# Kernel optimization log

Hardware: AMD Instinct MI355X
Metric: run time of the kernel (lower is better)

Reference implementation:

```python
import jax, jax.numpy as jnp
import numpy as np

HIDDEN = 2048
NUM_HEADS = 16
HEAD_DIM = HIDDEN // NUM_HEADS  # 128
ROPE_BASE = 10000.0


def setup_inputs() -> dict:
    key = jax.random.key(0)
    ks = jax.random.split(key, 5)
    B, T, C = 2, 2048, HIDDEN
    scale = 1.0 / np.sqrt(C)
    x = jax.random.normal(ks[0], (B, T, C), dtype=jnp.float32)
    Wq = jax.random.normal(ks[1], (C, C), dtype=jnp.float32) * scale
    Wk = jax.random.normal(ks[2], (C, C), dtype=jnp.float32) * scale
    Wv = jax.random.normal(ks[3], (C, C), dtype=jnp.float32) * scale
    Wo = jax.random.normal(ks[4], (C, C), dtype=jnp.float32) * scale
    return {"x": x, "Wq": Wq, "Wk": Wk, "Wv": Wv, "Wo": Wo}


def _rope_cos_sin(T, dtype):
    # inv_freq: [D/2]; emb: [T, D] = cat(freqs, freqs)
    inv_freq = 1.0 / (ROPE_BASE ** (jnp.arange(0, HEAD_DIM, 2, dtype=jnp.float32) / HEAD_DIM))
    t = jnp.arange(T, dtype=jnp.float32)
    freqs = t[:, None] * inv_freq[None, :]          # [T, D/2]
    emb = jnp.concatenate([freqs, freqs], axis=-1)  # [T, D]
    # broadcast shape [1, T, 1, D] to match q/k [B, T, H, D]
    return jnp.cos(emb)[None, :, None, :].astype(dtype), jnp.sin(emb)[None, :, None, :].astype(dtype)


def _rotate_half(u):
    u1, u2 = jnp.split(u, 2, axis=-1)
    return jnp.concatenate([-u2, u1], axis=-1)


def reference(x, Wq, Wk, Wv, Wo):
    B, T, C = x.shape
    H, D = NUM_HEADS, HEAD_DIM
    # QKV projections (torch Linear: x @ W.T). Weights here stored as [C, C] so use x @ W.
    q = (x @ Wq).reshape(B, T, H, D)
    k = (x @ Wk).reshape(B, T, H, D)
    v = (x @ Wv).reshape(B, T, H, D)
    cos, sin = _rope_cos_sin(T, x.dtype)
    q = q * cos + _rotate_half(q) * sin
    k = k * cos + _rotate_half(k) * sin
    # causal SDPA: scores [B, H, T, T]
    scale = 1.0 / jnp.sqrt(jnp.asarray(D, dtype=x.dtype))
    scores = jnp.einsum('bqhd,bkhd->bhqk', q, k) * scale
    causal = jnp.tril(jnp.ones((T, T), dtype=bool))
    scores = jnp.where(causal[None, None, :, :], scores, jnp.asarray(-jnp.inf, dtype=scores.dtype))
    attn = jax.nn.softmax(scores, axis=-1)
    out = jnp.einsum('bhqk,bkhd->bqhd', attn, v).reshape(B, T, C)
    return out @ Wo
```

## Files before the change

### kernel.cpp

```cpp
#include <hip/hip_runtime.h>
#include <hip/hip_bf16.h>

#define C_DIM 2048
#define NHEAD 16
#define HD 128
#define BB 2
#define TT 2048
#define MM (BB * TT)
#define NQT 32
#define N3 (3 * C_DIM)

typedef short short4v __attribute__((ext_vector_type(4)));
typedef short short8v __attribute__((ext_vector_type(8)));
typedef __bf16 bf16x4 __attribute__((ext_vector_type(4)));
typedef __bf16 bf16x8 __attribute__((ext_vector_type(8)));
typedef float f32x4 __attribute__((ext_vector_type(4)));

#define AS1 __attribute__((address_space(1)))
#define AS3 __attribute__((address_space(3)))

#define VMCNT(n) asm volatile("s_waitcnt vmcnt(" #n ")" ::: "memory")

__device__ __forceinline__ void load_lds16(const void* g, void* l) {
  __builtin_amdgcn_global_load_lds((const AS1 void*)g, (AS3 void*)l, 16, 0, 0);
}

__device__ __forceinline__ short f2bf(float f) {
  union { float f; unsigned u; } v; v.f = f;
  unsigned u = v.u;
  u += 0x7FFFu + ((u >> 16) & 1u);
  return (short)(u >> 16);
}
__device__ __forceinline__ float bf2f(short s) {
  union { unsigned u; float f; } v;
  v.u = ((unsigned)(unsigned short)s) << 16;
  return v.f;
}

__device__ __forceinline__ float exp2_fast(float x) {
  float r;
  asm("v_exp_f32 %0, %1" : "=v"(r) : "v"(x));
  return r;
}

__global__ __launch_bounds__(256) void cvt_x(const float* __restrict__ in,
                                             short* __restrict__ out, int n4) {
  int i = blockIdx.x * 256 + threadIdx.x;
  int stride = gridDim.x * 256;
  for (int idx = i; idx < n4; idx += stride) {
    float4 f = ((const float4*)in)[idx];
    short4v o;
    o[0] = f2bf(f.x); o[1] = f2bf(f.y); o[2] = f2bf(f.z); o[3] = f2bf(f.w);
    ((short4v*)out)[idx] = o;
  }
}

__global__ __launch_bounds__(256) void cvt_w_all(const float* __restrict__ Wq,
                                                 const float* __restrict__ Wk,
                                                 const float* __restrict__ Wv,
                                                 const float* __restrict__ Wo,
                                                 short* __restrict__ Wt) {
  __shared__ float tile[32][33];
  int z = blockIdx.z;
  const float* W = z == 0 ? Wq : z == 1 ? Wk : z == 2 ? Wv : Wo;
  short* dst = Wt + (size_t)z * C_DIM * C_DIM;
  int bx = blockIdx.x;
  int by = blockIdx.y;
  int lx = threadIdx.x & 31;
  int ly = threadIdx.x >> 5;
#pragma unroll
  for (int j = 0; j < 4; ++j) {
    int r = by * 32 + ly + j * 8;
    tile[ly + j * 8][lx] = W[(size_t)r * C_DIM + bx * 32 + lx];
  }
  __syncthreads();
#pragma unroll
  for (int j = 0; j < 4; ++j) {
    int n = bx * 32 + ly + j * 8;
    dst[(size_t)n * C_DIM + by * 32 + lx] = f2bf(tile[lx][ly + j * 8]);
  }
}

__global__ __launch_bounds__(256) void rope_tab(float2* __restrict__ tab) {
  int idx = blockIdx.x * 256 + threadIdx.x;
  int t = idx >> 6, d = idx & 63;
  float inv = expf(-9.210340371976184f * (float)d * (1.0f / 64.0f));
  float a = (float)t * inv;
  tab[idx] = make_float2(cosf(a), sinf(a));
}

template <int EPI>
__global__ __launch_bounds__(512, 4) void gemm8w(const short* __restrict__ A,
                                                 const short* __restrict__ Bt,
                                                 void* __restrict__ Cout,
                                                 int M, int N, int K, int NBN,
                                                 const float2* __restrict__ tab,
                                                 short* __restrict__ Qr,
                                                 short* __restrict__ Kr,
                                                 short* __restrict__ Vt) {
  __shared__ short smem[4 * 128 * 64];
  short (*sA)[128 * 64] = (short(*)[128 * 64])smem;
  short (*sB)[128 * 64] = (short(*)[128 * 64])(smem + 2 * 128 * 64);
  const int tid = threadIdx.x;
  const int lane = tid & 63;
  const int w = tid >> 6;
  const int wm = w >> 2, wn = w & 3;
  const int r = lane & 15, g = lane >> 4;

  const int wg = blockIdx.x;
  const int mb = wg / NBN, nb = wg % NBN;
  const int m0 = mb * 128, n0 = nb * 128;

  f32x4 acc[4][2] = {};

  auto stage = [&](int buf, int kt) {
#pragma unroll
    for (int j = 0; j < 2; ++j) {
      int p = j * 512 + tid;
      int row = p >> 3;
      int c16 = (p & 7) ^ (row & 7);
      load_lds16(A + (size_t)(m0 + row) * K + kt * 64 + c16 * 8,
                 &sA[buf][(j * 512 + w * 64) * 8]);
    }
#pragma unroll
    for (int j = 0; j < 2; ++j) {
      int p = j * 512 + tid;
      int row = p >> 3;
      int c16 = (p & 7) ^ (row & 7);
      load_lds16(Bt + (size_t)(n0 + row) * K + kt * 64 + c16 * 8,
                 &sB[buf][(j * 512 + w * 64) * 8]);
    }
  };

  auto compute = [&](int buf) {
#pragma unroll
    for (int kk = 0; kk < 2; ++kk) {
      bf16x8 af[4], bv[2];
#pragma unroll
      for (int m = 0; m < 4; ++m) {
        int row = wm * 64 + m * 16 + r;
        af[m] = *(const bf16x8*)((const char*)&sA[buf][0] + row * 128 +
                                 (((kk * 4 + g) ^ (row & 7)) << 4));
      }
#pragma unroll
      for (int n = 0; n < 2; ++n) {
        int row = wn * 32 + n * 16 + r;
        bv[n] = *(const bf16x8*)((const char*)&sB[buf][0] + row * 128 +
                                 (((kk * 4 + g) ^ (row & 7)) << 4));
      }
      __builtin_amdgcn_s_setprio(1);
#pragma unroll
      for (int m = 0; m < 4; ++m)
#pragma unroll
        for (int n = 0; n < 2; ++n)
          acc[m][n] = __builtin_amdgcn_mfma_f32_16x16x32_bf16(af[m], bv[n], acc[m][n], 0, 0, 0);
      __builtin_amdgcn_s_setprio(0);
    }
  };

  const int NT = K >> 6;
  stage(0, 0);
  stage(1, 1);
  VMCNT(4);
  __builtin_amdgcn_s_barrier();

  for (int t = 0; t < NT; ++t) {
    const int cur = t & 1;
    compute(cur);
    if (t + 1 < NT) {
      asm volatile("" ::: "memory");
      __builtin_amdgcn_s_barrier();
      if (t + 2 < NT) {
        stage(cur, t + 2);
        VMCNT(4);
      } else {
        VMCNT(0);
      }
      asm volatile("" ::: "memory");
      __builtin_amdgcn_s_barrier();
    }
  }

  if constexpr (EPI == 1) {
#pragma unroll
    for (int m = 0; m < 4; ++m)
#pragma unroll
      for (int n = 0; n < 2; ++n)
#pragma unroll
        for (int q = 0; q < 4; ++q) {
          int row = m0 + wm * 64 + m * 16 + g * 4 + q;
          int col = n0 + wn * 32 + n * 16 + r;
          ((float*)Cout)[(size_t)row * N + col] = acc[m][n][q];
        }
  } else {
    __syncthreads();
    short* S = smem;
#pragma unroll
    for (int m = 0; m < 4; ++m)
#pragma unroll
      for (int n = 0; n < 2; ++n)
#pragma unroll
        for (int q = 0; q < 4; ++q) {
          int row = wm * 64 + m * 16 + g * 4 + q;
          int col = wn * 32 + n * 16 + r;
          S[row * 130 + col] = f2bf(acc[m][n][q]);
        }
    __syncthreads();

    const int z = nb >> 4;
    const int h = nb & 15;
    const int b = m0 >> 11;
    const int bh = b * NHEAD + h;
    const int t_base = m0 & (TT - 1);

    if (z < 2) {
      short* dst = (z == 0) ? Qr : Kr;
      const float qs = (z == 0) ? 0.12751744f : 1.0f;
#pragma unroll
      for (int i = 0; i < 4; ++i) {
        int c = i * 512 + tid;
        int row = c >> 4;
        int d0 = (c & 15) * 8;
        int t = t_base + row;
        bool hi = d0 >= 64;
        int dbase = d0 & 63;
        short8v ov;
#pragma unroll
        for (int jj = 0; jj < 8; ++jj) {
          float u  = bf2f(S[row * 130 + d0 + jj]);
          float pu = bf2f(S[row * 130 + ((d0 + jj + 64) & 127)]);
          float2 cs = tab[(size_t)t * 64 + dbase + jj];
          float val = hi ? (u * cs.x + pu * cs.y) : (u * cs.x - pu * cs.y);
          ov[jj] = f2bf(val * qs);
        }
        *(short8v*)(dst + ((size_t)bh * TT + t) * HD + d0) = ov;
      }
    } else {
#pragma unroll
      for (int i = 0; i < 4; ++i) {
        int c = i * 512 + tid;
        int d = c >> 4;
        int tc = (c & 15) * 8;
        short8v ov;
#pragma unroll
        for (int jj = 0; jj < 8; ++jj) ov[jj] = S[(tc + jj) * 130 + d];
        *(short8v*)(Vt + ((size_t)bh * HD + d) * TT + t_base + tc) = ov;
      }
    }
  }
}

__global__ __launch_bounds__(256, 3) void attn_one(const short* __restrict__ Qr,
                                                   const short* __restrict__ Kr,
                                                   const short* __restrict__ Vt,
                                                   short* __restrict__ AO) {
  const int bx = blockIdx.x;
  const int j = bx >> 5, bh = bx & 31;
  const int qt = (j & 1) ? (j >> 1) : (NQT - 1 - (j >> 1));
  const int b = bh >> 4, h = bh & 15;
  const int tid = threadIdx.x;
  const int lane = tid & 63;
  const int w = tid >> 6;
  const int r = lane & 15, g = lane >> 4;

  __shared__ short sK[64 * 128];
  __shared__ short sV[128 * 64];
  __shared__ short sP[4][16 * 64];

  bf16x8 qf[4];
  {
    const short* qbp = Qr + ((size_t)bh * TT + qt * 64 + w * 16 + r) * HD + g * 8;
#pragma unroll
    for (int s = 0; s < 4; ++s) qf[s] = *(const bf16x8*)(qbp + s * 32);
  }

  f32x4 o[8] = {};
  float m = -1e30f, l = 0.f;

  short8v kreg[4], vreg[4];
  auto stage_load = [&](int kt) {
#pragma unroll
    for (int i = 0; i < 4; ++i) {
      int c = i * 256 + tid;
      kreg[i] = *(const short8v*)(Kr + ((size_t)bh * TT + kt * 64 + (c >> 4)) * HD + (c & 15) * 8);
    }
#pragma unroll
    for (int i = 0; i < 4; ++i) {
      int c = i * 256 + tid;
      vreg[i] = *(const short8v*)(Vt + ((size_t)bh * HD + (c >> 3)) * TT + kt * 64 + (c & 7) * 8);
    }
  };
  auto stage_write = [&]() {
#pragma unroll
    for (int i = 0; i < 4; ++i) {
      int c = i * 256 + tid;
      int row = c >> 4, cc = c & 15;
      int addr = (row * 256 + cc * 16) ^ ((row & 7) << 4);
      *(short8v*)((char*)sK + addr) = kreg[i];
    }
#pragma unroll
    for (int i = 0; i < 4; ++i) {
      int c = i * 256 + tid;
      int row = c >> 3, cc = c & 7;
      int addr = (row * 128 + cc * 16) ^ ((row & 7) << 4);
      *(short8v*)((char*)sV + addr) = vreg[i];
    }
  };

  char* pw = (char*)&sP[w][0];

  stage_load(0);
  stage_write();
  __syncthreads();

  for (int kt = 0; kt <= qt; ++kt) {
    f32x4 sacc[4] = {};
    __builtin_amdgcn_s_setprio(1);
#pragma unroll
    for (int nf = 0; nf < 4; ++nf) {
#pragma unroll
      for (int ss = 0; ss < 4; ++ss) {
        int krow = nf * 16 + r;
        int addr = (krow * 256 + (ss * 32 + g * 8) * 2) ^ ((krow & 7) << 4);
        bf16x8 kf = *(const bf16x8*)((char*)sK + addr);
        sacc[nf] = __builtin_amdgcn_mfma_f32_16x16x32_bf16(kf, qf[ss], sacc[nf], 0, 0, 0);
      }
    }
    __builtin_amdgcn_s_setprio(0);

    if (kt < qt) stage_load(kt + 1);

    if (kt == qt) {
#pragma unroll
      for (int nf = 0; nf < 4; ++nf)
#pragma unroll
        for (int q = 0; q < 4; ++q)
          if (nf * 16 + g * 4 + q > w * 16 + r) sacc[nf][q] = -1e30f;
    }

    float p01 = fmaxf(fmaxf(sacc[0][0], sacc[0][1]), fmaxf(sacc[0][2], sacc[0][3]));
    float p23 = fmaxf(fmaxf(sacc[1][0], sacc[1][1]), fmaxf(sacc[1][2], sacc[1][3]));
    float p45 = fmaxf(fmaxf(sacc[2][0], sacc[2][1]), fmaxf(sacc[2][2], sacc[2][3]));
    float p67 = fmaxf(fmaxf(sacc[3][0], sacc[3][1]), fmaxf(sacc[3][2], sacc[3][3]));
    float pmax = fmaxf(fmaxf(p01, p23), fmaxf(p45, p67));
    pmax = fmaxf(pmax, __shfl_xor(pmax, 16, 64));
    pmax = fmaxf(pmax, __shfl_xor(pmax, 32, 64));

    if (!__all(pmax - m <= 8.0f)) {
      float mnew = fmaxf(m, pmax);
      float alpha = exp2_fast(m - mnew);
      m = mnew;
      l *= alpha;
#pragma unroll
      for (int q = 0; q < 4; ++q) {
        float aq = __shfl(alpha, (g * 4 + q) | (lane & 48), 64);
#pragma unroll
        for (int nf2 = 0; nf2 < 8; ++nf2) o[nf2][q] *= aq;
      }
    }

    float s16 = 0.f;
#pragma unroll
    for (int nf = 0; nf < 4; ++nf) {
      f32x4 pe;
#pragma unroll
      for (int q = 0; q < 4; ++q) pe[q] = exp2_fast(sacc[nf][q] - m);
      s16 += (pe[0] + pe[1]) + (pe[2] + pe[3]);
      int addr = (r * 128 + nf * 32 + g * 8) ^ ((r & 7) << 4);
      *(bf16x4*)(pw + addr) = __builtin_convertvector(pe, bf16x4);
    }
    float rs = s16;
    rs += __shfl_xor(rs, 16, 64);
    rs += __shfl_xor(rs, 32, 64);
    l += rs;

    __builtin_amdgcn_s_setprio(1);
#pragma unroll
    for (int s2 = 0; s2 < 2; ++s2) {
      int paddr = (r * 128 + s2 * 64 + g * 16) ^ ((r & 7) << 4);
      bf16x8 pa = *(const bf16x8*)(pw + paddr);
#pragma unroll
      for (int nf2 = 0; nf2 < 8; ++nf2) {
        int drow = nf2 * 16 + r;
        int addr = (drow * 128 + (s2 * 32 + g * 8) * 2) ^ ((drow & 7) << 4);
        bf16x8 vb = *(const bf16x8*)((char*)sV + addr);
        o[nf2] = __builtin_amdgcn_mfma_f32_16x16x32_bf16(pa, vb, o[nf2], 0, 0, 0);
      }
    }
    __builtin_amdgcn_s_setprio(0);

    __syncthreads();
    if (kt < qt) {
      stage_write();
      __syncthreads();
    }
  }

  float linv = 1.0f / l;
  float lrow[4];
#pragma unroll
  for (int q = 0; q < 4; ++q)
    lrow[q] = __shfl(linv, (g * 4 + q) | (lane & 48), 64);
  short* ow = sK + w * 16 * 128;
#pragma unroll
  for (int nf2 = 0; nf2 < 8; ++nf2)
#pragma unroll
    for (int q = 0; q < 4; ++q)
      ow[(g * 4 + q) * 128 + nf2 * 16 + r] = f2bf(o[nf2][q] * lrow[q]);
  __syncthreads();

#pragma unroll
  for (int ch = 0; ch < 4; ++ch) {
    int c = ch * 256 + tid;
    int orow = c >> 4;
    int ocol = (c & 15) * 8;
    int t = qt * 64 + orow;
    *(short8v*)(AO + ((size_t)b * TT + t) * C_DIM + h * HD + ocol) =
        *(const short8v*)(sK + orow * 128 + ocol);
  }
}

extern "C" void kernel_launch(void* const* d_in, const int* in_sizes, int n_in,
                              void* d_out, int out_size, void* d_ws, size_t ws_size,
                              hipStream_t stream) {
  const float* x  = (const float*)d_in[0];
  const float* Wq = (const float*)d_in[1];
  const float* Wk = (const float*)d_in[2];
  const float* Wv = (const float*)d_in[3];
  const float* Wo = (const float*)d_in[4];

  char* ws = (char*)d_ws;
  size_t off = 0;
  auto take = [&](size_t bytes) {
    char* p = ws + off;
    off += (bytes + 255) & ~(size_t)255;
    return p;
  };
  const size_t xe = (size_t)MM * C_DIM;
  const size_t we = (size_t)C_DIM * C_DIM;
  short* xb   = (short*)take(xe * 2);
  short* wqkv = (short*)take(4 * we * 2);
  short* wot  = wqkv + 3 * we;
  short* Qr   = (short*)take(xe * 2);
  short* Kr   = (short*)take(xe * 2);
  short* Vtr  = (short*)take(xe * 2);
  short* AO   = (short*)take(xe * 2);
  float2* tab = (float2*)take((size_t)TT * 64 * sizeof(float2));

  cvt_x<<<2048, 256, 0, stream>>>(x, xb, (int)(xe / 4));
  cvt_w_all<<<dim3(64, 64, 4), 256, 0, stream>>>(Wq, Wk, Wv, Wo, wqkv);
  rope_tab<<<(TT * 64) / 256, 256, 0, stream>>>(tab);

  gemm8w<2><<<1536, 512, 0, stream>>>(xb, wqkv, nullptr, MM, N3, C_DIM, N3 / 128,
                                      tab, Qr, Kr, Vtr);

  attn_one<<<1024, 256, 0, stream>>>(Qr, Kr, Vtr, AO);

  gemm8w<1><<<512, 512, 0, stream>>>(AO, wot, d_out, MM, C_DIM, C_DIM, C_DIM / 128,
                                     nullptr, nullptr, nullptr, nullptr);
}
```

Baseline: 264.5 us.

## Load K/V tiles directly into LDS via global_load_lds, raise occupancy to 4

Replaces the register-staged K/V prefetch (global load into registers during compute, then LDS store) with direct global-to-LDS loads. The XOR swizzle moves from the LDS address to the global source address. This frees the kreg/vreg registers, which allows launch bounds of 4 waves per SIMD. The cost is that the next tile's load no longer overlaps the current tile's compute: it is issued after the barrier and waited on with vmcnt(0), so the kernel relies on the extra occupancy to hide that latency.

After: 281.4 us. +6.4%, slower.

```diff
diff --git a/kernel.cpp b/kernel.cpp
--- a/kernel.cpp
+++ b/kernel.cpp
@@ -250,7 +250,7 @@
   }
 }
 
-__global__ __launch_bounds__(256, 3) void attn_one(const short* __restrict__ Qr,
+__global__ __launch_bounds__(256, 4) void attn_one(const short* __restrict__ Qr,
                                                    const short* __restrict__ Kr,
                                                    const short* __restrict__ Vt,
                                                    short* __restrict__ AO) {
@@ -277,40 +277,29 @@
   f32x4 o[8] = {};
   float m = -1e30f, l = 0.f;
 
-  short8v kreg[4], vreg[4];
-  auto stage_load = [&](int kt) {
-#pragma unroll
-    for (int i = 0; i < 4; ++i) {
-      int c = i * 256 + tid;
-      kreg[i] = *(const short8v*)(Kr + ((size_t)bh * TT + kt * 64 + (c >> 4)) * HD + (c & 15) * 8);
-    }
-#pragma unroll
-    for (int i = 0; i < 4; ++i) {
-      int c = i * 256 + tid;
-      vreg[i] = *(const short8v*)(Vt + ((size_t)bh * HD + (c >> 3)) * TT + kt * 64 + (c & 7) * 8);
-    }
-  };
-  auto stage_write = [&]() {
+  const short* Kbase = Kr + (size_t)bh * TT * HD;
+  const short* Vbase = Vt + (size_t)bh * HD * TT;
+  auto stage_lds = [&](int kt) {
 #pragma unroll
     for (int i = 0; i < 4; ++i) {
       int c = i * 256 + tid;
       int row = c >> 4, cc = c & 15;
-      int addr = (row * 256 + cc * 16) ^ ((row & 7) << 4);
-      *(short8v*)((char*)sK + addr) = kreg[i];
+      load_lds16(Kbase + (size_t)(kt * 64 + row) * HD + (cc ^ (row & 7)) * 8,
+                 (char*)sK + c * 16);
     }
 #pragma unroll
     for (int i = 0; i < 4; ++i) {
       int c = i * 256 + tid;
       int row = c >> 3, cc = c & 7;
-      int addr = (row * 128 + cc * 16) ^ ((row & 7) << 4);
-      *(short8v*)((char*)sV + addr) = vreg[i];
+      load_lds16(Vbase + (size_t)row * TT + kt * 64 + (cc ^ (row & 7)) * 8,
+                 (char*)sV + c * 16);
     }
   };
 
   char* pw = (char*)&sP[w][0];
 
-  stage_load(0);
-  stage_write();
+  stage_lds(0);
+  VMCNT(0);
   __syncthreads();
 
   for (int kt = 0; kt <= qt; ++kt) {
@@ -327,8 +316,6 @@
       }
     }
     __builtin_amdgcn_s_setprio(0);
-
-    if (kt < qt) stage_load(kt + 1);
 
     if (kt == qt) {
 #pragma unroll
@@ -391,7 +378,8 @@
 
     __syncthreads();
     if (kt < qt) {
-      stage_write();
+      stage_lds(kt + 1);
+      VMCNT(0);
       __syncthreads();
     }
   }
```
